# Optimization experiments

Hardware: AMD Instinct MI355X
Metric: run time of the kernel (lower is better)

Reference implementation:

```python
import jax, jax.numpy as jnp
import numpy as np

EPS = 1e-12


def setup_inputs() -> dict:
    key = jax.random.key(0)
    n, k, Eu, iterations = 200_000, 7, 1_600_000, 3
    k1, k2, k3 = jax.random.split(key, 3)
    # undirected edge list; each undirected edge yields two directed edges
    su = jax.random.randint(k1, (Eu,), 0, n, dtype=jnp.int32)
    du = jax.random.randint(k2, (Eu,), 0, n, dtype=jnp.int32)
    src = jnp.concatenate([su, du])                                   # [E]
    dst = jnp.concatenate([du, su])                                   # [E]
    rev = jnp.concatenate([jnp.arange(Eu, 2 * Eu, dtype=jnp.int32),
                           jnp.arange(Eu, dtype=jnp.int32)])          # [E]
    # node priors (rows sum to 1), mimicking the soft label priors
    prior = jax.random.uniform(k3, (n, k), minval=0.1, maxval=1.0)
    prior = prior / prior.sum(axis=1, keepdims=True)
    # label-to-label potential: log(beta) on the diagonal (beta = 3.0)
    W = jnp.log(3.0) * jnp.eye(k, dtype=jnp.float32)
    return {"prior": prior, "W": W, "src": src, "dst": dst,
            "rev": rev, "iterations": iterations}


def reference(prior, W, src, dst, rev, iterations):
    n, k = prior.shape
    E = src.shape[0]
    psi = jnp.exp(jnp.clip(W, -10.0, 10.0))                           # [k,k]
    msgs = jnp.full((E, k), 1.0 / k, dtype=prior.dtype)

    def step(msgs, _):
        # product of incoming messages per node, in log-space (msgs >= EPS)
        logm = jnp.log(msgs)                                          # [E,k]
        logP = jax.ops.segment_sum(logm, dst, num_segments=n)         # [n,k]
        # per directed edge (i -> j): remove reverse message j -> i
        prod_in_i = jnp.exp(logP[src] - logm[rev])                    # [E,k]
        b = jnp.maximum(prior[src] * prod_in_i, EPS)                  # [E,k]
        m_new = jnp.maximum(b @ psi, EPS)                             # [E,k]
        m_new = m_new / jnp.maximum(m_new.sum(-1, keepdims=True), EPS)
        return m_new, None

    msgs, _ = jax.lax.scan(step, msgs, None, length=int(iterations))

    # beliefs
    logP = jax.ops.segment_sum(jnp.log(msgs), dst, num_segments=n)    # [n,k]
    b = jnp.maximum(prior * jnp.exp(logP), EPS)
    return b / jnp.maximum(b.sum(-1, keepdims=True), EPS)
```

## Files before the change

kernel.cpp:

```cpp
#include <hip/hip_runtime.h>
#include <hip/hip_bf16.h>
#include <hip/hip_fp16.h>

#define K 7
#define EPSF 1e-12f
#define LOG_INV_K (-1.9459101090932196f)
#define LOG7 1.9459101090932196f
#define LOG2_EPS (-39.8631371f)
#define LN2 0.69314718056f
#define INV_LN2 1.44269504f
#define SBN 512
#define SBSH 9
#define NSBMAX 768
#define PB 256
#define CAP 16

__device__ __forceinline__ float ldf(const void* p, size_t idx, int mode) {
    return mode ? ((const float*)p)[idx]
                : __bfloat162float(((const __hip_bfloat16*)p)[idx]);
}

__device__ __forceinline__ void load_psi(const void* W, float* psi, int mode) {
    if (threadIdx.x < K * K) {
        float w = ldf(W, threadIdx.x, mode);
        w = fminf(fmaxf(w, -10.f), 10.f);
        psi[threadIdx.x] = __expf(w);
    }
    __syncthreads();
}

__device__ __forceinline__ void bp_lin(const float* b, const float* psi, float* m) {
    float o[K], sum = 0.f;
#pragma unroll
    for (int j = 0; j < K; j++) {
        float acc = 0.f;
#pragma unroll
        for (int i = 0; i < K; i++) acc += b[i] * psi[i * K + j];
        o[j] = fmaxf(acc, EPSF);
        sum += o[j];
    }
    float inv = __fdividef(1.f, fmaxf(sum, EPSF));
#pragma unroll
    for (int j = 0; j < K; j++) m[j] = o[j] * inv;
}

__device__ __forceinline__ void acc_log_msg(const float* b, const float* psi, float* acc) {
    float m[K];
    bp_lin(b, psi, m);
#pragma unroll
    for (int j = 0; j < K; j++) acc[j] += __logf(m[j]);
}

__device__ __forceinline__ void dec_pd(uint4 w, float* p, int* degv, int* u1) {
    p[0] = __uint_as_float((w.x & 0xffffu) << 16);
    p[1] = __uint_as_float(w.x & 0xffff0000u);
    p[2] = __uint_as_float((w.y & 0xffffu) << 16);
    p[3] = __uint_as_float(w.y & 0xffff0000u);
    p[4] = __uint_as_float((w.z & 0xffffu) << 16);
    p[5] = __uint_as_float(w.z & 0xffff0000u);
    p[6] = __uint_as_float((w.w & 0xffffu) << 16);
    *degv = (int)((w.w >> 16) & 0x7fffu);
    *u1 = (int)(w.w >> 31);
}

__device__ __forceinline__ unsigned short f2h(float f) {
    __half h = __float2half_rn(f);
    return *reinterpret_cast<unsigned short*>(&h);
}
__device__ __forceinline__ float h2f(unsigned short u) {
    __half h;
    *reinterpret_cast<unsigned short*>(&h) = u;
    return __half2float(h);
}
__device__ __forceinline__ uint4 pack7h(const float* m, int E) {
    uint4 r;
    r.x = (unsigned)f2h(m[0]) | ((unsigned)f2h(m[1]) << 16);
    r.y = (unsigned)f2h(m[2]) | ((unsigned)f2h(m[3]) << 16);
    r.z = (unsigned)f2h(m[4]) | ((unsigned)f2h(m[5]) << 16);
    r.w = (unsigned)f2h(m[6]) | ((unsigned)(E & 0xffff) << 16);
    return r;
}
__device__ __forceinline__ int unpack7h(uint4 w, float* m) {
    m[0] = h2f((unsigned short)(w.x & 0xffffu));
    m[1] = h2f((unsigned short)(w.x >> 16));
    m[2] = h2f((unsigned short)(w.y & 0xffffu));
    m[3] = h2f((unsigned short)(w.y >> 16));
    m[4] = h2f((unsigned short)(w.z & 0xffffu));
    m[5] = h2f((unsigned short)(w.z >> 16));
    m[6] = h2f((unsigned short)(w.w & 0xffffu));
    return (int)(short)(w.w >> 16);
}
__device__ __forceinline__ signed char clampE(int E) {
    return (signed char)(E < -120 ? -120 : (E > 120 ? 120 : E));
}

__global__ void sniff11_kernel(const void* __restrict__ W, int* __restrict__ prm,
                               int* __restrict__ btot, int NSB) {
    if (blockIdx.x != 0) return;
    for (int i = threadIdx.x; i < NSB; i += 64) btot[i] = 0;
    if (threadIdx.x != 0) return;
    const unsigned int* Wraw = (const unsigned int*)W;
    int mode = ((Wraw[0] >> 16) != 0u) ? 1 : 0;
    float diag0 = 0.f, offd0 = 0.f;
    int structured = 1;
    for (int i = 0; i < K; i++)
        for (int j = 0; j < K; j++) {
            float w = ldf(W, i * K + j, mode);
            w = fminf(fmaxf(w, -10.f), 10.f);
            float e = __expf(w);
            if (i == 0 && j == 0) diag0 = e;
            if (i == 0 && j == 1) offd0 = e;
            if (i == j) { if (i > 0 && e != diag0) structured = 0; }
            else       { if (!(i == 0 && j == 1) && e != offd0) structured = 0; }
        }
    if (!(offd0 >= 0.2f) || !(diag0 >= offd0)) structured = 0;
    prm[0] = mode | (structured << 1);
    ((float*)prm)[1] = offd0;
    ((float*)prm)[2] = diag0;
}

__global__ void hist6_kernel(const int* __restrict__ dst, int* __restrict__ hist,
                             int* __restrict__ btot, int E, int EPB, int NSB) {
    __shared__ int h[NSBMAX];
    for (int i = threadIdx.x; i < NSB; i += 256) h[i] = 0;
    __syncthreads();
    int blk = blockIdx.x;
    int e0 = blk * EPB, e1 = min(e0 + EPB, E);
    for (int e = e0 + (int)threadIdx.x; e < e1; e += 256)
        atomicAdd(&h[dst[e] >> SBSH], 1);
    __syncthreads();
    for (int i = threadIdx.x; i < NSB; i += 256) {
        int c = h[i];
        hist[i * PB + blk] = c;
        if (c) atomicAdd(&btot[i], c);
    }
}

__global__ void bscan6_kernel(const int* __restrict__ btot, int* __restrict__ boff, int NSB) {
    __shared__ int s[1024];
    int t = threadIdx.x;
    int x = (t < NSB) ? btot[t] : 0;
    s[t] = x;
    __syncthreads();
    for (int o = 1; o < 1024; o <<= 1) {
        int y = (t >= o) ? s[t - o] : 0;
        __syncthreads();
        s[t] += y;
        __syncthreads();
    }
    if (t < NSB) boff[t] = s[t] - x;
    if (t == NSB - 1) boff[NSB] = s[t];
}

__global__ void sscan6_kernel(const int* __restrict__ hist, const int* __restrict__ boff,
                              int* __restrict__ woff) {
    __shared__ int s[PB];
    int b = blockIdx.x, t = threadIdx.x;
    int x = hist[b * PB + t];
    s[t] = x;
    __syncthreads();
    for (int o = 1; o < PB; o <<= 1) {
        int y = (t >= o) ? s[t - o] : 0;
        __syncthreads();
        s[t] += y;
        __syncthreads();
    }
    woff[b * PB + t] = boff[b] + s[t] - x;
}

__global__ void part6_kernel(const int* __restrict__ src, const int* __restrict__ dst,
                             const int* __restrict__ woff, unsigned int* __restrict__ coarse,
                             int E, int EPB, int NSB) {
    __shared__ int cur[NSBMAX];
    int blk = blockIdx.x;
    for (int i = threadIdx.x; i < NSB; i += 256) cur[i] = woff[i * PB + blk];
    __syncthreads();
    int e0 = blk * EPB, e1 = min(e0 + EPB, E);
    for (int e = e0 + (int)threadIdx.x; e < e1; e += 256) {
        int d = dst[e];
        int b = d >> SBSH;
        unsigned int pk = (unsigned int)src[e] | ((unsigned int)(d & (SBN - 1)) << 18);
        int pos = atomicAdd(&cur[b], 1);
        coarse[pos] = pk;
    }
}

__global__ void cfill9_kernel(const unsigned int* __restrict__ coarse,
                              const int* __restrict__ boff,
                              const void* __restrict__ prior, const int* __restrict__ prm,
                              int* __restrict__ cur, int* __restrict__ nbr,
                              uint4* __restrict__ PD, int n) {
    __shared__ int lcnt[SBN], lcur[SBN];
    int b = blockIdx.x, t = threadIdx.x;
    int mode = prm[0] & 1;
    for (int i = t; i < SBN; i += 256) lcnt[i] = 0;
    __syncthreads();
    int s0 = boff[b], s1 = boff[b + 1];
    for (int i = s0 + t; i < s1; i += 256)
        atomicAdd(&lcnt[coarse[i] >> 18], 1);
    __syncthreads();
    if (t == 0) {
        int a = s0;
        for (int l = 0; l < SBN; l++) { lcur[l] = a; a += lcnt[l]; }
    }
    __syncthreads();
    int v0 = b << SBSH;
    for (int i = t; i < SBN; i += 256) {
        int v = v0 + i;
        if (v >= n) continue;
        int degv = lcnt[i];
        cur[v] = lcur[i] + degv;
        unsigned int pb[K];
        float p[K];
        if (mode == 0) {
            const unsigned short* pr = (const unsigned short*)prior;
#pragma unroll
            for (int j = 0; j < K; j++) {
                pb[j] = pr[(size_t)v * K + j];
                p[j] = __uint_as_float(pb[j] << 16);
            }
        } else {
            const float* pr = (const float*)prior;
#pragma unroll
            for (int j = 0; j < K; j++) {
                p[j] = pr[(size_t)v * K + j];
                __hip_bfloat16 hh = __float2bfloat16(p[j]);
                pb[j] = *(unsigned short*)&hh;
            }
        }
        float es = __expf((float)(degv - 1) * LOG_INV_K);
        float mx = p[0];
#pragma unroll
        for (int j = 1; j < K; j++) mx = fmaxf(mx, p[j]);
        unsigned int u1 = (mx * es <= EPSF) ? 1u : 0u;
        int dcap = degv > 0x7fff ? 0x7fff : degv;
        uint4 w;
        w.x = pb[0] | (pb[1] << 16);
        w.y = pb[2] | (pb[3] << 16);
        w.z = pb[4] | (pb[5] << 16);
        w.w = pb[6] | (((unsigned int)dcap) << 16) | (u1 << 31);
        PD[v] = w;
    }
    __syncthreads();
    for (int i = s0 + t; i < s1; i += 256) {
        unsigned int w = coarse[i];
        int pos = atomicAdd(&lcur[w >> 18], 1);
        nbr[pos] = (int)(w & 0x3FFFFu);
    }
}

__global__ void mbuild11_kernel(const uint4* __restrict__ PD, const void* __restrict__ W,
                                const int* __restrict__ prm, uint4* __restrict__ M1h, int n) {
    __shared__ float psi[K * K];
    int pm = prm[0];
    int mode = pm & 1, strq = (pm >> 1) & 1;
    float offd = ((const float*)prm)[1], diag = ((const float*)prm)[2];
    load_psi(W, psi, mode);
    int v = blockIdx.x * blockDim.x + threadIdx.x;
    if (v >= n) return;
    float p[K]; int dv, u1v;
    dec_pd(PD[v], p, &dv, &u1v);
    float es = __expf((float)(dv - 1) * LOG_INV_K);
    float b[K], S = 0.f;
#pragma unroll
    for (int i = 0; i < K; i++) { b[i] = fmaxf(p[i] * es, EPSF); S += b[i]; }
    float m1n[K];
    if (strq) {
        float cb = diag - offd, norm = 6.f * offd + diag;
        float sc = __fdividef(7.f, S * norm);
#pragma unroll
        for (int i = 0; i < K; i++) m1n[i] = (offd * S + cb * b[i]) * sc;
    } else {
        float m1[K];
        bp_lin(b, psi, m1);
#pragma unroll
        for (int i = 0; i < K; i++) m1n[i] = 7.f * m1[i];
    }
    M1h[v] = pack7h(m1n, 0);
}

__global__ void n2v12_kernel(const int* __restrict__ cur, const int* __restrict__ nbr,
                             const uint4* __restrict__ M1h, const uint4* __restrict__ PD,
                             const int* __restrict__ prm, uint4* __restrict__ LP1,
                             signed char* __restrict__ E1x, int n) {
    int t = blockIdx.x * blockDim.x + threadIdx.x;
    int v = t >> 2, qi = t & 3;
    if (v >= n) return;
    int start = v ? cur[v - 1] : 0, end = cur[v];
    int len = end - start;
    int lo = start + ((len * qi) >> 2), hi = start + ((len * (qi + 1)) >> 2);
    float acc[K] = {1.f, 1.f, 1.f, 1.f, 1.f, 1.f, 1.f};
    int e = lo;
    for (; e + 3 < hi; e += 4) {
        int u0 = nbr[e], u1 = nbr[e + 1], u2 = nbr[e + 2], u3 = nbr[e + 3];
        uint4 w0 = M1h[u0], w1 = M1h[u1], w2 = M1h[u2], w3 = M1h[u3];
        float a[K], b[K], c[K], d[K];
        unpack7h(w0, a); unpack7h(w1, b); unpack7h(w2, c); unpack7h(w3, d);
#pragma unroll
        for (int i = 0; i < K; i++) acc[i] *= (a[i] * b[i]) * (c[i] * d[i]);
    }
    for (; e < hi; e++) {
        float a[K];
        unpack7h(M1h[nbr[e]], a);
#pragma unroll
        for (int i = 0; i < K; i++) acc[i] *= fmaxf(a[i], 1e-30f);
    }
#pragma unroll
    for (int i = 0; i < K; i++) {
        acc[i] *= __shfl_xor(acc[i], 1, 64);
        acc[i] *= __shfl_xor(acc[i], 2, 64);
    }
    if (qi) return;
    float pv[K]; int dv, u1v;
    dec_pd(PD[v], pv, &dv, &u1v);
    float le[K], mx = -1e30f;
    float corr = (float)len * LOG7;
#pragma unroll
    for (int i = 0; i < K; i++) {
        le[i] = __logf(fmaxf(pv[i] * acc[i], 1e-37f)) - corr;
        mx = fmaxf(mx, le[i]);
    }
    int E1 = (int)ceilf(mx * INV_LN2);
    float fm[K];
#pragma unroll
    for (int i = 0; i < K; i++) fm[i] = __expf(le[i] - (float)E1 * LN2);
    LP1[v] = pack7h(fm, E1);
    E1x[v] = clampE(E1);
}

__global__ void n3v12_kernel(const int* __restrict__ cur, const int* __restrict__ nbr,
                             const uint4* __restrict__ PD, const uint4* __restrict__ LP1,
                             const signed char* __restrict__ E1x,
                             const void* __restrict__ W, const int* __restrict__ prm,
                             uint4* __restrict__ Q2h, signed char* __restrict__ E2x, int n) {
    __shared__ float psi[K * K];
    __shared__ int lively[256 * CAP];
    int pm = prm[0];
    int mode = pm & 1, strq = (pm >> 1) & 1;
    float offd = ((const float*)prm)[1], diag = ((const float*)prm)[2];
    load_psi(W, psi, mode);
    int t = blockIdx.x * blockDim.x + threadIdx.x;
    int v = t >> 2, qi = t & 3;
    if (v >= n) return;
    int start = v ? cur[v - 1] : 0, end = cur[v];
    int len = end - start;
    int lo = start + ((len * qi) >> 2), hi = start + ((len * (qi + 1)) >> 2);
    float cb = diag - offd, norm = 6.f * offd + diag;
    float pv[K]; int dv, u1v;
    dec_pd(PD[v], pv, &dv, &u1v);
    float rm1v[K];
    if (strq && u1v) {
#pragma unroll
        for (int i = 0; i < K; i++) rm1v[i] = 7.f;
    } else {
        float es = __expf((float)(dv - 1) * LOG_INV_K);
        float b1[K], S1 = 0.f;
#pragma unroll
        for (int i = 0; i < K; i++) { b1[i] = fmaxf(pv[i] * es, EPSF); S1 += b1[i]; }
        if (strq) {
            float inv = __fdividef(1.f, S1 * norm);
#pragma unroll
            for (int i = 0; i < K; i++)
                rm1v[i] = __fdividef(1.f, (offd * S1 + cb * b1[i]) * inv);
        } else {
            float m1[K];
            bp_lin(b1, psi, m1);
#pragma unroll
            for (int i = 0; i < K; i++) rm1v[i] = __fdividef(1.f, m1[i]);
        }
    }
    float acc[K];
    int cn = 0;
    if (strq) {
        float F = __fdividef(norm, offd) * 1.01f;
        int Ethr = (int)floorf(LOG2_EPS - log2f(F));
#pragma unroll
        for (int i = 0; i < K; i++) acc[i] = 1.f;
        auto proc = [&](uint4 q) {
            float m[K];
            int E = unpack7h(q, m);
            float b[K], S = 0.f;
#pragma unroll
            for (int i = 0; i < K; i++) {
                b[i] = fmaxf(ldexpf(m[i] * rm1v[i], E), EPSF);
                S += b[i];
            }
            float crS = __fdividef(cb, S);
#pragma unroll
            for (int i = 0; i < K; i++) acc[i] *= fmaf(crS, b[i], offd);
            cn++;
        };
        int base = (int)threadIdx.x * CAP;
        int cnt = 0;
        auto consider = [&](int u, int Eu) {
            if (Eu > Ethr) {
                if (cnt < CAP) lively[base + cnt++] = u;
                else proc(LP1[u]);
            }
        };
        int e = lo;
        for (; e + 3 < hi; e += 4) {
            int u0 = nbr[e], u1 = nbr[e + 1], u2 = nbr[e + 2], u3 = nbr[e + 3];
            int a0 = E1x[u0], a1 = E1x[u1], a2 = E1x[u2], a3 = E1x[u3];
            consider(u0, a0); consider(u1, a1); consider(u2, a2); consider(u3, a3);
        }
        for (; e < hi; e++) { int u = nbr[e]; consider(u, (int)E1x[u]); }
        for (int j = 0; j < cnt; j++) proc(LP1[lively[base + j]]);
#pragma unroll
        for (int i = 0; i < K; i++) {
            acc[i] *= __shfl_xor(acc[i], 1, 64);
            acc[i] *= __shfl_xor(acc[i], 2, 64);
        }
    } else {
#pragma unroll
        for (int i = 0; i < K; i++) acc[i] = 0.f;
        for (int e = lo; e < hi; e++) {
            float m[K];
            int E = unpack7h(LP1[nbr[e]], m);
            float b[K];
#pragma unroll
            for (int i = 0; i < K; i++)
                b[i] = fmaxf(ldexpf(m[i] * rm1v[i], E), EPSF);
            acc_log_msg(b, psi, acc);
        }
#pragma unroll
        for (int i = 0; i < K; i++) {
            acc[i] += __shfl_xor(acc[i], 1, 64);
            acc[i] += __shfl_xor(acc[i], 2, 64);
        }
    }
    cn += __shfl_xor(cn, 1, 64);
    cn += __shfl_xor(cn, 2, 64);
    if (qi) return;
    float le2[K], mx = -1e30f;
    if (strq) {
        float corr = (float)cn * __logf(norm) + (float)(len - cn) * LOG7;
#pragma unroll
        for (int i = 0; i < K; i++) {
            le2[i] = __logf(fmaxf(pv[i] * acc[i], 1e-37f)) - corr;
            mx = fmaxf(mx, le2[i]);
        }
    } else {
#pragma unroll
        for (int i = 0; i < K; i++) {
            le2[i] = __logf(fmaxf(pv[i], 1e-37f)) + acc[i];
            mx = fmaxf(mx, le2[i]);
        }
    }
    int E2 = (int)ceilf(mx * INV_LN2);
    float fm[K];
#pragma unroll
    for (int i = 0; i < K; i++) fm[i] = __expf(le2[i] - (float)E2 * LN2);
    Q2h[v] = pack7h(fm, E2);
    E2x[v] = clampE(E2);
}

__global__ void n4v12_kernel(const int* __restrict__ cur, const int* __restrict__ nbr,
                             const uint4* __restrict__ M1h, const uint4* __restrict__ Q2h,
                             const signed char* __restrict__ E2x,
                             const uint4* __restrict__ LP1, const void* __restrict__ prior,
                             const void* __restrict__ W, const int* __restrict__ prm,
                             void* __restrict__ out, int n) {
    __shared__ float psi[K * K];
    __shared__ int lively[256 * CAP];
    int pm = prm[0];
    int mode = pm & 1, strq = (pm >> 1) & 1;
    float offd = ((const float*)prm)[1], diag = ((const float*)prm)[2];
    load_psi(W, psi, mode);
    int t = blockIdx.x * blockDim.x + threadIdx.x;
    int v = t >> 2, qi = t & 3;
    if (v >= n) return;
    int start = v ? cur[v - 1] : 0, end = cur[v];
    int len = end - start;
    int lo = start + ((len * qi) >> 2), hi = start + ((len * (qi + 1)) >> 2);
    float cb = diag - offd, norm = 6.f * offd + diag;
    float e1v[K];
    {
        float m[K];
        int E1 = unpack7h(LP1[v], m);
#pragma unroll
        for (int i = 0; i < K; i++) e1v[i] = ldexpf(m[i], E1);
    }
    float acc[K];
    int cn = 0;
    if (strq) {
        float mx1 = e1v[0];
#pragma unroll
        for (int i = 1; i < K; i++) mx1 = fmaxf(mx1, e1v[i]);
        float F = __fdividef(norm, offd) * 1.01f;
        int m2u = (F * mx1 <= EPSF);
        int Ethr = (int)floorf(LOG2_EPS - log2f(F));
#pragma unroll
        for (int i = 0; i < K; i++) acc[i] = 1.f;
        auto proc2u = [&](int u) {
            float m[K];
            int E2 = unpack7h(Q2h[u], m);
            float b3[K], S = 0.f;
#pragma unroll
            for (int i = 0; i < K; i++) {
                b3[i] = fmaxf(ldexpf(m[i] * 7.f, E2), EPSF);
                S += b3[i];
            }
            float crS = __fdividef(cb, S);
#pragma unroll
            for (int i = 0; i < K; i++) acc[i] *= fmaf(crS, b3[i], offd);
            cn++;
        };
        auto procGen = [&](int u) {
            float m[K];
            int E2 = unpack7h(Q2h[u], m);
            float tt[K];
            unpack7h(M1h[u], tt);
            float b2[K], S2 = 0.f;
#pragma unroll
            for (int i = 0; i < K; i++) {
                b2[i] = fmaxf(e1v[i] * __fdividef(7.f, tt[i]), EPSF);
                S2 += b2[i];
            }
            float inv2 = __fdividef(1.f, S2 * norm);
            float b3[K], S3 = 0.f;
#pragma unroll
            for (int i = 0; i < K; i++) {
                float m2v = (offd * S2 + cb * b2[i]) * inv2;
                float e2 = ldexpf(m[i], E2);
                b3[i] = fmaxf(__fdividef(e2, m2v), EPSF);
                S3 += b3[i];
            }
            float crS3 = __fdividef(cb, S3);
#pragma unroll
            for (int i = 0; i < K; i++) acc[i] *= fmaf(crS3, b3[i], offd);
            cn++;
        };
        int base = (int)threadIdx.x * CAP;
        int cnt = 0;
        auto consider = [&](int u, int Eu) {
            if (Eu > Ethr) {
                if (cnt < CAP) lively[base + cnt++] = u;
                else { if (m2u) proc2u(u); else procGen(u); }
            }
        };
        int e = lo;
        for (; e + 3 < hi; e += 4) {
            int u0 = nbr[e], u1 = nbr[e + 1], u2 = nbr[e + 2], u3 = nbr[e + 3];
            int a0 = E2x[u0], a1 = E2x[u1], a2 = E2x[u2], a3 = E2x[u3];
            consider(u0, a0); consider(u1, a1); consider(u2, a2); consider(u3, a3);
        }
        for (; e < hi; e++) { int u = nbr[e]; consider(u, (int)E2x[u]); }
        if (m2u) { for (int j = 0; j < cnt; j++) proc2u(lively[base + j]); }
        else     { for (int j = 0; j < cnt; j++) procGen(lively[base + j]); }
#pragma unroll
        for (int i = 0; i < K; i++) {
            acc[i] *= __shfl_xor(acc[i], 1, 64);
            acc[i] *= __shfl_xor(acc[i], 2, 64);
        }
    } else {
#pragma unroll
        for (int i = 0; i < K; i++) acc[i] = 0.f;
        for (int e = lo; e < hi; e++) {
            int u = nbr[e];
            uint4 q = Q2h[u];
            float m[K];
            int E2 = unpack7h(q, m);
            float tt[K];
            unpack7h(M1h[u], tt);
            float b2[K];
#pragma unroll
            for (int i = 0; i < K; i++)
                b2[i] = fmaxf(e1v[i] * __fdividef(7.f, fmaxf(tt[i], 1e-30f)), EPSF);
            float m2[K];
            bp_lin(b2, psi, m2);
            float b3[K];
#pragma unroll
            for (int i = 0; i < K; i++) {
                float e2 = ldexpf(m[i], E2);
                b3[i] = fmaxf(__fdividef(e2, m2[i]), EPSF);
            }
            acc_log_msg(b3, psi, acc);
        }
#pragma unroll
        for (int i = 0; i < K; i++) {
            acc[i] += __shfl_xor(acc[i], 1, 64);
            acc[i] += __shfl_xor(acc[i], 2, 64);
        }
    }
    cn += __shfl_xor(cn, 1, 64);
    cn += __shfl_xor(cn, 2, 64);
    if (qi) return;
    float bb[K], sum = 0.f;
    if (strq) {
        float corr = (float)cn * __logf(norm) + (float)(len - cn) * LOG7;
#pragma unroll
        for (int i = 0; i < K; i++) {
            float p = ldf(prior, (size_t)v * K + i, mode);
            bb[i] = fmaxf(__expf(__logf(fmaxf(p * acc[i], 1e-37f)) - corr), EPSF);
            sum += bb[i];
        }
    } else {
#pragma unroll
        for (int i = 0; i < K; i++) {
            float p = ldf(prior, (size_t)v * K + i, mode);
            bb[i] = fmaxf(p * __expf(acc[i]), EPSF);
            sum += bb[i];
        }
    }
    float inv = __fdividef(1.f, fmaxf(sum, EPSF));
#pragma unroll
    for (int i = 0; i < K; i++) {
        float val = bb[i] * inv;
        if (mode) ((float*)out)[(size_t)v * K + i] = val;
        else ((__hip_bfloat16*)out)[(size_t)v * K + i] = __float2bfloat16(val);
    }
}

__device__ __forceinline__ void bp_msg(const float* b, const float* psi, float* lm) {
    float m[K];
    bp_lin(b, psi, m);
#pragma unroll
    for (int j = 0; j < K; j++) lm[j] = __logf(m[j]);
}
__device__ __forceinline__ void msg1(const void* prior, int node, int degv, int mode,
                                     const float* psi, float* lm) {
    float es = __expf((float)(degv - 1) * LOG_INV_K);
    float b[K];
#pragma unroll
    for (int i = 0; i < K; i++)
        b[i] = fmaxf(ldf(prior, (size_t)node * K + i, mode) * es, EPSF);
    bp_msg(b, psi, lm);
}
__device__ __forceinline__ void msgF(const void* prior, int node,
                                     const float* __restrict__ logP,
                                     const float* lmrev, int mode,
                                     const float* psi, float* lm) {
    float b[K];
#pragma unroll
    for (int i = 0; i < K; i++)
        b[i] = fmaxf(ldf(prior, (size_t)node * K + i, mode) *
                     __expf(logP[(size_t)node * K + i] - lmrev[i]), EPSF);
    bp_msg(b, psi, lm);
}
__global__ void deg_kernel(const int* __restrict__ su, const int* __restrict__ du,
                           int* __restrict__ deg, int Eu) {
    int u = blockIdx.x * blockDim.x + threadIdx.x;
    if (u >= Eu) return;
    atomicAdd(&deg[su[u]], 1);
    atomicAdd(&deg[du[u]], 1);
}
__global__ void pass1_kernel(const int* __restrict__ su, const int* __restrict__ du,
                             const int* __restrict__ deg, const void* __restrict__ prior,
                             const void* __restrict__ W, const int* __restrict__ prm,
                             float* __restrict__ logP1, int Eu) {
    __shared__ float psi[K * K];
    int mode = prm[0] & 1;
    load_psi(W, psi, mode);
    int u = blockIdx.x * blockDim.x + threadIdx.x;
    if (u >= Eu) return;
    int s = su[u], d = du[u];
    float lm[K];
    msg1(prior, s, deg[s], mode, psi, lm);
#pragma unroll
    for (int j = 0; j < K; j++) atomicAdd(&logP1[(size_t)d * K + j], lm[j]);
    msg1(prior, d, deg[d], mode, psi, lm);
#pragma unroll
    for (int j = 0; j < K; j++) atomicAdd(&logP1[(size_t)s * K + j], lm[j]);
}
__global__ void pass2_kernel(const int* __restrict__ su, const int* __restrict__ du,
                             const int* __restrict__ deg, const void* __restrict__ prior,
                             const void* __restrict__ W, const int* __restrict__ prm,
                             const float* __restrict__ logP1, float* __restrict__ logP2, int Eu) {
    __shared__ float psi[K * K];
    int mode = prm[0] & 1;
    load_psi(W, psi, mode);
    int u = blockIdx.x * blockDim.x + threadIdx.x;
    if (u >= Eu) return;
    int s = su[u], d = du[u];
    float lm1sd[K], lm1ds[K], lm[K];
    msg1(prior, s, deg[s], mode, psi, lm1sd);
    msg1(prior, d, deg[d], mode, psi, lm1ds);
    msgF(prior, s, logP1, lm1ds, mode, psi, lm);
#pragma unroll
    for (int j = 0; j < K; j++) atomicAdd(&logP2[(size_t)d * K + j], lm[j]);
    msgF(prior, d, logP1, lm1sd, mode, psi, lm);
#pragma unroll
    for (int j = 0; j < K; j++) atomicAdd(&logP2[(size_t)s * K + j], lm[j]);
}
__global__ void pass3_kernel(const int* __restrict__ su, const int* __restrict__ du,
                             const int* __restrict__ deg, const void* __restrict__ prior,
                             const void* __restrict__ W, const int* __restrict__ prm,
                             const float* __restrict__ logP1, const float* __restrict__ logP2,
                             float* __restrict__ logP3, int Eu) {
    __shared__ float psi[K * K];
    int mode = prm[0] & 1;
    load_psi(W, psi, mode);
    int u = blockIdx.x * blockDim.x + threadIdx.x;
    if (u >= Eu) return;
    int s = su[u], d = du[u];
    float lm1sd[K], lm1ds[K], lm2sd[K], lm2ds[K], lm[K];
    msg1(prior, s, deg[s], mode, psi, lm1sd);
    msg1(prior, d, deg[d], mode, psi, lm1ds);
    msgF(prior, s, logP1, lm1ds, mode, psi, lm2sd);
    msgF(prior, d, logP1, lm1sd, mode, psi, lm2ds);
    msgF(prior, s, logP2, lm2ds, mode, psi, lm);
#pragma unroll
    for (int j = 0; j < K; j++) atomicAdd(&logP3[(size_t)d * K + j], lm[j]);
    msgF(prior, d, logP2, lm2sd, mode, psi, lm);
#pragma unroll
    for (int j = 0; j < K; j++) atomicAdd(&logP3[(size_t)s * K + j], lm[j]);
}
__global__ void belief_kernel(const float* __restrict__ logP3, const void* __restrict__ prior,
                              const int* __restrict__ prm, void* __restrict__ out, int n) {
    int v = blockIdx.x * blockDim.x + threadIdx.x;
    if (v >= n) return;
    int mode = prm[0] & 1;
    float b[K], sum = 0.f;
#pragma unroll
    for (int j = 0; j < K; j++) {
        b[j] = fmaxf(ldf(prior, (size_t)v * K + j, mode) * __expf(logP3[(size_t)v * K + j]), EPSF);
        sum += b[j];
    }
    float inv = __fdividef(1.f, fmaxf(sum, EPSF));
#pragma unroll
    for (int j = 0; j < K; j++) {
        float val = b[j] * inv;
        if (mode) ((float*)out)[(size_t)v * K + j] = val;
        else ((__hip_bfloat16*)out)[(size_t)v * K + j] = __float2bfloat16(val);
    }
}

extern "C" void kernel_launch(void* const* d_in, const int* in_sizes, int n_in,
                              void* d_out, int out_size, void* d_ws, size_t ws_size,
                              hipStream_t stream) {
    const void* prior = d_in[0];
    const void* W     = d_in[1];
    const int* src = (const int*)d_in[2];
    const int* dst = (const int*)d_in[3];

    int n  = in_sizes[0] / K;
    int E  = in_sizes[2];
    int Eu = E / 2;

    const int B = 256;
    int gn  = (n + B - 1) / B;
    int gn4 = (4 * n + B - 1) / B;
    int ge  = (Eu + B - 1) / B;

    int NSB = (n + SBN - 1) >> SBSH;
    int EPB = (E + PB - 1) / PB;

    char* ws = (char*)d_ws;
    size_t off = 0;
    auto alloc = [&](size_t bytes) { size_t o = off; off = (off + bytes + 127) & ~(size_t)127; return o; };

    size_t xsz = (size_t)E * 4;
    if ((size_t)n * 48 > xsz) xsz = (size_t)n * 48;
    size_t o_nbr  = alloc((size_t)E * 4);
    size_t o_X    = alloc(xsz);
    size_t o_PD   = alloc((size_t)n * 16);
    size_t o_E1x  = alloc((size_t)n);
    size_t o_E2x  = alloc((size_t)n);
    size_t o_cur  = alloc((size_t)n * 4);
    size_t o_hist = alloc((size_t)NSB * PB * 4);
    size_t o_woff = alloc((size_t)NSB * PB * 4);
    size_t o_boff = alloc((size_t)(NSB + 1) * 4);
    size_t o_btot = alloc((size_t)NSB * 4);
    size_t o_prm  = alloc(64);
    size_t need_v12 = off;

    bool v12_ok = (ws_size >= need_v12) && (n <= (1 << 18)) && (NSB <= NSBMAX) && (NSB >= 1);

    if (v12_ok) {
        int*   nbr    = (int*)(ws + o_nbr);
        unsigned int* coarse = (unsigned int*)(ws + o_X);
        uint4* LP1    = (uint4*)(ws + o_X);
        uint4* Q2h    = (uint4*)(ws + o_X + (size_t)n * 16);
        uint4* M1h    = (uint4*)(ws + o_X + (size_t)n * 32);
        uint4* PD     = (uint4*)(ws + o_PD);
        signed char* E1x = (signed char*)(ws + o_E1x);
        signed char* E2x = (signed char*)(ws + o_E2x);
        int*   cur    = (int*)(ws + o_cur);
        int*   hist   = (int*)(ws + o_hist);
        int*   woff   = (int*)(ws + o_woff);
        int*   boff   = (int*)(ws + o_boff);
        int*   btot   = (int*)(ws + o_btot);
        int*   prm    = (int*)(ws + o_prm);

        sniff11_kernel<<<1, 64, 0, stream>>>(W, prm, btot, NSB);
        hist6_kernel<<<PB, B, 0, stream>>>(dst, hist, btot, E, EPB, NSB);
        bscan6_kernel<<<1, 1024, 0, stream>>>(btot, boff, NSB);
        sscan6_kernel<<<NSB, PB, 0, stream>>>(hist, boff, woff);
        part6_kernel<<<PB, B, 0, stream>>>(src, dst, woff, coarse, E, EPB, NSB);
        cfill9_kernel<<<NSB, B, 0, stream>>>(coarse, boff, prior, prm, cur, nbr, PD, n);
        mbuild11_kernel<<<gn, B, 0, stream>>>(PD, W, prm, M1h, n);
        n2v12_kernel<<<gn4, B, 0, stream>>>(cur, nbr, M1h, PD, prm, LP1, E1x, n);
        n3v12_kernel<<<gn4, B, 0, stream>>>(cur, nbr, PD, LP1, E1x, W, prm, Q2h, E2x, n);
        n4v12_kernel<<<gn4, B, 0, stream>>>(cur, nbr, M1h, Q2h, E2x, LP1, prior, W, prm,
                                            d_out, n);
        return;
    }

    {
        float* logP1 = (float*)d_ws;
        float* logP2 = logP1 + (size_t)n * K;
        float* logP3 = logP2 + (size_t)n * K;
        int*   deg   = (int*)(logP3 + (size_t)n * K);
        int*   prm   = deg + n;
        int*   btot  = prm + 8;
        sniff11_kernel<<<1, 64, 0, stream>>>(W, prm, btot, 0);
        hipMemsetAsync(d_ws, 0, ((size_t)3 * n * K + n) * sizeof(float), stream);
        deg_kernel<<<ge, B, 0, stream>>>(src, dst, deg, Eu);
        pass1_kernel<<<ge, B, 0, stream>>>(src, dst, deg, prior, W, prm, logP1, Eu);
        pass2_kernel<<<ge, B, 0, stream>>>(src, dst, deg, prior, W, prm, logP1, logP2, Eu);
        pass3_kernel<<<ge, B, 0, stream>>>(src, dst, deg, prior, W, prm, logP1, logP2, logP3, Eu);
        belief_kernel<<<gn, B, 0, stream>>>(logP3, prior, prm, d_out, n);
    }
}
```

Measured before the change: 287.9 us.

## Fuse message build into CSR fill and transpose lively-list shared layout

Moves the first-message construction from a separate kernel into the CSR fill kernel, so the per-node M1h values are computed while the prior and degree are still in registers. This saves one launch and a re-read of PD. M1h gets its own workspace slot because the coarse buffer that previously hosted it is still being read during the fill. The per-thread lively candidate list in n3/n4 is halved and stored column-major (index*256+lane), which removes shared-memory bank conflicts and cuts LDS use, but more candidates fall back to immediate processing.

```diff
diff --git a/kernel.cpp b/kernel.cpp
--- a/kernel.cpp
+++ b/kernel.cpp
@@ -13,7 +13,7 @@
 #define SBSH 9
 #define NSBMAX 768
 #define PB 256
-#define CAP 16
+#define CAP 8
 
 __device__ __forceinline__ float ldf(const void* p, size_t idx, int mode) {
     return mode ? ((const float*)p)[idx]
@@ -185,14 +185,19 @@
     }
 }
 
-__global__ void cfill9_kernel(const unsigned int* __restrict__ coarse,
-                              const int* __restrict__ boff,
-                              const void* __restrict__ prior, const int* __restrict__ prm,
-                              int* __restrict__ cur, int* __restrict__ nbr,
-                              uint4* __restrict__ PD, int n) {
+__global__ void cfill13_kernel(const unsigned int* __restrict__ coarse,
+                               const int* __restrict__ boff,
+                               const void* __restrict__ prior, const void* __restrict__ W,
+                               const int* __restrict__ prm,
+                               int* __restrict__ cur, int* __restrict__ nbr,
+                               uint4* __restrict__ PD, uint4* __restrict__ M1h, int n) {
     __shared__ int lcnt[SBN], lcur[SBN];
+    __shared__ float psi[K * K];
     int b = blockIdx.x, t = threadIdx.x;
-    int mode = prm[0] & 1;
+    int pm = prm[0];
+    int mode = pm & 1, strq = (pm >> 1) & 1;
+    float offd = ((const float*)prm)[1], diag = ((const float*)prm)[2];
+    load_psi(W, psi, mode);
     for (int i = t; i < SBN; i += 256) lcnt[i] = 0;
     __syncthreads();
     int s0 = boff[b], s1 = boff[b + 1];
@@ -240,6 +245,22 @@
         w.z = pb[4] | (pb[5] << 16);
         w.w = pb[6] | (((unsigned int)dcap) << 16) | (u1 << 31);
         PD[v] = w;
+        float bb[K], S = 0.f;
+#pragma unroll
+        for (int j = 0; j < K; j++) { bb[j] = fmaxf(p[j] * es, EPSF); S += bb[j]; }
+        float m1n[K];
+        if (strq) {
+            float cb = diag - offd, norm = 6.f * offd + diag;
+            float sc = __fdividef(7.f, S * norm);
+#pragma unroll
+            for (int j = 0; j < K; j++) m1n[j] = (offd * S + cb * bb[j]) * sc;
+        } else {
+            float m1[K];
+            bp_lin(bb, psi, m1);
+#pragma unroll
+            for (int j = 0; j < K; j++) m1n[j] = 7.f * m1[j];
+        }
+        M1h[v] = pack7h(m1n, 0);
     }
     __syncthreads();
     for (int i = s0 + t; i < s1; i += 256) {
@@ -247,36 +268,6 @@
         int pos = atomicAdd(&lcur[w >> 18], 1);
         nbr[pos] = (int)(w & 0x3FFFFu);
     }
-}
-
-__global__ void mbuild11_kernel(const uint4* __restrict__ PD, const void* __restrict__ W,
-                                const int* __restrict__ prm, uint4* __restrict__ M1h, int n) {
-    __shared__ float psi[K * K];
-    int pm = prm[0];
-    int mode = pm & 1, strq = (pm >> 1) & 1;
-    float offd = ((const float*)prm)[1], diag = ((const float*)prm)[2];
-    load_psi(W, psi, mode);
-    int v = blockIdx.x * blockDim.x + threadIdx.x;
-    if (v >= n) return;
-    float p[K]; int dv, u1v;
-    dec_pd(PD[v], p, &dv, &u1v);
-    float es = __expf((float)(dv - 1) * LOG_INV_K);
-    float b[K], S = 0.f;
-#pragma unroll
-    for (int i = 0; i < K; i++) { b[i] = fmaxf(p[i] * es, EPSF); S += b[i]; }
-    float m1n[K];
-    if (strq) {
-        float cb = diag - offd, norm = 6.f * offd + diag;
-        float sc = __fdividef(7.f, S * norm);
-#pragma unroll
-        for (int i = 0; i < K; i++) m1n[i] = (offd * S + cb * b[i]) * sc;
-    } else {
-        float m1[K];
-        bp_lin(b, psi, m1);
-#pragma unroll
-        for (int i = 0; i < K; i++) m1n[i] = 7.f * m1[i];
-    }
-    M1h[v] = pack7h(m1n, 0);
 }
 
 __global__ void n2v12_kernel(const int* __restrict__ cur, const int* __restrict__ nbr,
@@ -328,7 +319,7 @@
     E1x[v] = clampE(E1);
 }
 
-__global__ void n3v12_kernel(const int* __restrict__ cur, const int* __restrict__ nbr,
+__global__ void n3v13_kernel(const int* __restrict__ cur, const int* __restrict__ nbr,
                              const uint4* __restrict__ PD, const uint4* __restrict__ LP1,
                              const signed char* __restrict__ E1x,
                              const void* __restrict__ W, const int* __restrict__ prm,
@@ -390,11 +381,11 @@
             for (int i = 0; i < K; i++) acc[i] *= fmaf(crS, b[i], offd);
             cn++;
         };
-        int base = (int)threadIdx.x * CAP;
+        int lane = (int)threadIdx.x;
         int cnt = 0;
         auto consider = [&](int u, int Eu) {
             if (Eu > Ethr) {
-                if (cnt < CAP) lively[base + cnt++] = u;
+                if (cnt < CAP) lively[cnt++ * 256 + lane] = u;
                 else proc(LP1[u]);
             }
         };
@@ -405,7 +396,7 @@
             consider(u0, a0); consider(u1, a1); consider(u2, a2); consider(u3, a3);
         }
         for (; e < hi; e++) { int u = nbr[e]; consider(u, (int)E1x[u]); }
-        for (int j = 0; j < cnt; j++) proc(LP1[lively[base + j]]);
+        for (int j = 0; j < cnt; j++) proc(LP1[lively[j * 256 + lane]]);
 #pragma unroll
         for (int i = 0; i < K; i++) {
             acc[i] *= __shfl_xor(acc[i], 1, 64);
@@ -455,7 +446,7 @@
     E2x[v] = clampE(E2);
 }
 
-__global__ void n4v12_kernel(const int* __restrict__ cur, const int* __restrict__ nbr,
+__global__ void n4v13_kernel(const int* __restrict__ cur, const int* __restrict__ nbr,
                              const uint4* __restrict__ M1h, const uint4* __restrict__ Q2h,
                              const signed char* __restrict__ E2x,
                              const uint4* __restrict__ LP1, const void* __restrict__ prior,
@@ -531,11 +522,11 @@
             for (int i = 0; i < K; i++) acc[i] *= fmaf(crS3, b3[i], offd);
             cn++;
         };
-        int base = (int)threadIdx.x * CAP;
+        int lane = (int)threadIdx.x;
         int cnt = 0;
         auto consider = [&](int u, int Eu) {
             if (Eu > Ethr) {
-                if (cnt < CAP) lively[base + cnt++] = u;
+                if (cnt < CAP) lively[cnt++ * 256 + lane] = u;
                 else { if (m2u) proc2u(u); else procGen(u); }
             }
         };
@@ -546,8 +537,8 @@
             consider(u0, a0); consider(u1, a1); consider(u2, a2); consider(u3, a3);
         }
         for (; e < hi; e++) { int u = nbr[e]; consider(u, (int)E2x[u]); }
-        if (m2u) { for (int j = 0; j < cnt; j++) proc2u(lively[base + j]); }
-        else     { for (int j = 0; j < cnt; j++) procGen(lively[base + j]); }
+        if (m2u) { for (int j = 0; j < cnt; j++) proc2u(lively[j * 256 + lane]); }
+        else     { for (int j = 0; j < cnt; j++) procGen(lively[j * 256 + lane]); }
 #pragma unroll
         for (int i = 0; i < K; i++) {
             acc[i] *= __shfl_xor(acc[i], 1, 64);
@@ -751,10 +742,11 @@
     auto alloc = [&](size_t bytes) { size_t o = off; off = (off + bytes + 127) & ~(size_t)127; return o; };
 
     size_t xsz = (size_t)E * 4;
-    if ((size_t)n * 48 > xsz) xsz = (size_t)n * 48;
+    if ((size_t)n * 32 > xsz) xsz = (size_t)n * 32;
     size_t o_nbr  = alloc((size_t)E * 4);
     size_t o_X    = alloc(xsz);
     size_t o_PD   = alloc((size_t)n * 16);
+    size_t o_M1h  = alloc((size_t)n * 16);
     size_t o_E1x  = alloc((size_t)n);
     size_t o_E2x  = alloc((size_t)n);
     size_t o_cur  = alloc((size_t)n * 4);
@@ -763,17 +755,17 @@
     size_t o_boff = alloc((size_t)(NSB + 1) * 4);
     size_t o_btot = alloc((size_t)NSB * 4);
     size_t o_prm  = alloc(64);
-    size_t need_v12 = off;
-
-    bool v12_ok = (ws_size >= need_v12) && (n <= (1 << 18)) && (NSB <= NSBMAX) && (NSB >= 1);
-
-    if (v12_ok) {
+    size_t need_v13 = off;
+
+    bool v13_ok = (ws_size >= need_v13) && (n <= (1 << 18)) && (NSB <= NSBMAX) && (NSB >= 1);
+
+    if (v13_ok) {
         int*   nbr    = (int*)(ws + o_nbr);
         unsigned int* coarse = (unsigned int*)(ws + o_X);
         uint4* LP1    = (uint4*)(ws + o_X);
         uint4* Q2h    = (uint4*)(ws + o_X + (size_t)n * 16);
-        uint4* M1h    = (uint4*)(ws + o_X + (size_t)n * 32);
         uint4* PD     = (uint4*)(ws + o_PD);
+        uint4* M1h    = (uint4*)(ws + o_M1h);
         signed char* E1x = (signed char*)(ws + o_E1x);
         signed char* E2x = (signed char*)(ws + o_E2x);
         int*   cur    = (int*)(ws + o_cur);
@@ -788,11 +780,11 @@
         bscan6_kernel<<<1, 1024, 0, stream>>>(btot, boff, NSB);
         sscan6_kernel<<<NSB, PB, 0, stream>>>(hist, boff, woff);
         part6_kernel<<<PB, B, 0, stream>>>(src, dst, woff, coarse, E, EPB, NSB);
-        cfill9_kernel<<<NSB, B, 0, stream>>>(coarse, boff, prior, prm, cur, nbr, PD, n);
-        mbuild11_kernel<<<gn, B, 0, stream>>>(PD, W, prm, M1h, n);
+        cfill13_kernel<<<NSB, B, 0, stream>>>(coarse, boff, prior, W, prm, cur, nbr,
+                                              PD, M1h, n);
         n2v12_kernel<<<gn4, B, 0, stream>>>(cur, nbr, M1h, PD, prm, LP1, E1x, n);
-        n3v12_kernel<<<gn4, B, 0, stream>>>(cur, nbr, PD, LP1, E1x, W, prm, Q2h, E2x, n);
-        n4v12_kernel<<<gn4, B, 0, stream>>>(cur, nbr, M1h, Q2h, E2x, LP1, prior, W, prm,
+        n3v13_kernel<<<gn4, B, 0, stream>>>(cur, nbr, PD, LP1, E1x, W, prm, Q2h, E2x, n);
+        n4v13_kernel<<<gn4, B, 0, stream>>>(cur, nbr, M1h, Q2h, E2x, LP1, prior, W, prm,
                                             d_out, n);
         return;
     }
```

Measured after the change: 289.1 us, median of 2. About the same (+0.4%).
